# Performance work log

Hardware: AMD Instinct MI355X
Metric: run time of the kernel (lower is better)

## Reference

```python
import jax, jax.numpy as jnp
import numpy as np

E, I, H, T = 8, 2816, 1024, 8192

def setup_inputs() -> dict:
    key = jax.random.key(0)
    ks = jax.random.split(key, 5)
    scale_w = 1.0 / np.sqrt(H)
    return {
        "hidden_states": jax.random.normal(ks[0], (T, H), jnp.float32),
        "router_logits": jax.random.normal(ks[1], (T, E), jnp.float32),
        "W1": jax.random.normal(ks[2], (E, I, H), jnp.float32) * scale_w,
        "W3": jax.random.normal(ks[3], (E, I, H), jnp.float32) * scale_w,
        "W2": jax.random.normal(ks[4], (E, H, I), jnp.float32) * (1.0 / np.sqrt(I)),
        "top_k": 2,
    }

def reference(hidden_states, router_logits, W1, W3, W2, top_k):
    # softmax router in fp32, topk, renormalize (renormalize=True, use_grouped_topk=False)
    probs = jax.nn.softmax(router_logits.astype(jnp.float32), axis=-1)  # [T,E]
    vals, idx = jax.lax.top_k(probs, top_k)                             # [T,K]
    vals = vals / jnp.sum(vals, axis=-1, keepdims=True)
    vals = vals.astype(hidden_states.dtype)
    n_tok, n_exp = probs.shape
    # dense per-token expert weight matrix [T,E]; zero for unrouted experts,
    # mathematically identical to the gather/scatter-add in the ipex op
    w = jnp.zeros((n_tok, n_exp), hidden_states.dtype).at[
        jnp.arange(n_tok)[:, None], idx].add(vals)

    def expert_step(acc, args):
        We1, We3, We2, we = args  # [I,H], [I,H], [H,I], [T]
        h = jax.nn.silu(hidden_states @ We1.T) * (hidden_states @ We3.T)  # [T,I]
        return acc + we[:, None] * (h @ We2.T), None

    out, _ = jax.lax.scan(expert_step, jnp.zeros_like(hidden_states),
                          (W1, W3, W2, w.T))
    return out
```

## Files before the change

### kernel.cpp

```cpp
#include <hip/hip_runtime.h>
#include <stdint.h>

#define NE 8
#define NI 2816
#define NH 1024
#define NT 8192
#define NPAIR (NT * 2)

typedef __bf16 bf16x8 __attribute__((ext_vector_type(8)));
typedef float f32x4 __attribute__((ext_vector_type(4)));

__device__ __forceinline__ uint16_t f2bf(float f) {
    union { float f; uint32_t u; } v;
    v.f = f;
    return (uint16_t)((v.u + 0x7FFFu + ((v.u >> 16) & 1u)) >> 16);
}

__device__ __forceinline__ float bflo(uint32_t u) {
    union { uint32_t x; float f; } v; v.x = u << 16; return v.f;
}
__device__ __forceinline__ float bfhi(uint32_t u) {
    union { uint32_t x; float f; } v; v.x = u & 0xffff0000u; return v.f;
}

__device__ __forceinline__ void gld16(const void* g, void* l) {
    __builtin_amdgcn_global_load_lds(
        (__attribute__((address_space(1))) void*)(uintptr_t)g,
        (__attribute__((address_space(3))) void*)(uint32_t)(uintptr_t)l,
        16, 0, 0);
}

__global__ __launch_bounds__(256) void k_cvt_w13(const float* __restrict__ W1,
                                                 const float* __restrict__ W3,
                                                 uint16_t* __restrict__ Wg) {
    int row = blockIdx.x * 2 + (threadIdx.x >> 7);
    int g = threadIdx.x & 127;
    const float* src = (blockIdx.y == 0) ? W1 : W3;
    int e = row / NI;
    int r = row - e * NI;
    size_t drow = (size_t)e * (2 * NI) + (size_t)((r >> 4) * 32 + (r & 15) + (blockIdx.y ? 16 : 0));
    const float4* sp = (const float4*)(src + (size_t)row * NH);
    float4 a = sp[g * 2];
    float4 b = sp[g * 2 + 1];
    uint4 o;
    o.x = (uint32_t)f2bf(a.x) | ((uint32_t)f2bf(a.y) << 16);
    o.y = (uint32_t)f2bf(a.z) | ((uint32_t)f2bf(a.w) << 16);
    o.z = (uint32_t)f2bf(b.x) | ((uint32_t)f2bf(b.y) << 16);
    o.w = (uint32_t)f2bf(b.z) | ((uint32_t)f2bf(b.w) << 16);
    ((uint4*)(Wg + drow * NH))[g] = o;
}

__global__ __launch_bounds__(256) void k_cvt_flat(const float* __restrict__ S,
                                                  uint16_t* __restrict__ D) {
    size_t i = (size_t)blockIdx.x * 256 + threadIdx.x;
    float4 a = ((const float4*)S)[i * 2];
    float4 b = ((const float4*)S)[i * 2 + 1];
    uint4 o;
    o.x = (uint32_t)f2bf(a.x) | ((uint32_t)f2bf(a.y) << 16);
    o.y = (uint32_t)f2bf(a.z) | ((uint32_t)f2bf(a.w) << 16);
    o.z = (uint32_t)f2bf(b.x) | ((uint32_t)f2bf(b.y) << 16);
    o.w = (uint32_t)f2bf(b.z) | ((uint32_t)f2bf(b.w) << 16);
    ((uint4*)D)[i] = o;
}

__global__ __launch_bounds__(256) void k_router(const float* __restrict__ logits,
                                                int* __restrict__ tok_e,
                                                float2* __restrict__ tok_w,
                                                int* __restrict__ counts) {
    int t = blockIdx.x * 256 + threadIdx.x;
    if (t >= NT) return;
    float4 a = ((const float4*)logits)[(size_t)t * 2];
    float4 b = ((const float4*)logits)[(size_t)t * 2 + 1];
    float l[8] = {a.x, a.y, a.z, a.w, b.x, b.y, b.z, b.w};
    int i0 = 0; float l0 = l[0];
#pragma unroll
    for (int e = 1; e < 8; e++) if (l[e] > l0) { l0 = l[e]; i0 = e; }
    int i1 = -1; float l1 = -3.4e38f;
#pragma unroll
    for (int e = 0; e < 8; e++) if (e != i0 && l[e] > l1) { l1 = l[e]; i1 = e; }
    float w0 = 1.f / (1.f + __expf(l1 - l0));
    float w1 = 1.f - w0;
    tok_e[t] = i0 | (i1 << 8);
    tok_w[t] = make_float2(w0, w1);
    atomicAdd(&counts[i0], 1);
    atomicAdd(&counts[i1], 1);
}

__global__ void k_scan(const int* __restrict__ counts, int* __restrict__ offsets,
                       int* __restrict__ cursor) {
    if (threadIdx.x == 0) {
        int o = 0;
        for (int e = 0; e < NE; e++) { offsets[e] = o; cursor[e] = o; o += counts[e]; }
    }
}

__global__ __launch_bounds__(128) void k_gather(const float* __restrict__ x,
                                                const int* __restrict__ tok_e,
                                                const float2* __restrict__ tok_w,
                                                int* __restrict__ cursor,
                                                uint16_t* __restrict__ Xg,
                                                int2* __restrict__ tok_slots,
                                                float* __restrict__ slot_w) {
    int t = blockIdx.x;
    __shared__ int ss[2];
    if (threadIdx.x == 0) {
        int ee = tok_e[t];
        float2 w = tok_w[t];
        int s0 = atomicAdd(&cursor[ee & 0xff], 1);
        int s1 = atomicAdd(&cursor[(ee >> 8) & 0xff], 1);
        ss[0] = s0; ss[1] = s1;
        tok_slots[t] = make_int2(s0, s1);
        slot_w[s0] = w.x;
        slot_w[s1] = w.y;
    }
    __syncthreads();
    int s0 = ss[0], s1 = ss[1];
    int i = threadIdx.x;
    const float4* xr = (const float4*)(x + (size_t)t * NH);
    float4 a = xr[i * 2];
    float4 b = xr[i * 2 + 1];
    uint4 o;
    o.x = (uint32_t)f2bf(a.x) | ((uint32_t)f2bf(a.y) << 16);
    o.y = (uint32_t)f2bf(a.z) | ((uint32_t)f2bf(a.w) << 16);
    o.z = (uint32_t)f2bf(b.x) | ((uint32_t)f2bf(b.y) << 16);
    o.w = (uint32_t)f2bf(b.z) | ((uint32_t)f2bf(b.w) << 16);
    ((uint4*)(Xg + (size_t)s0 * NH))[i] = o;
    ((uint4*)(Xg + (size_t)s1 * NH))[i] = o;
}


#define BAR()  asm volatile("s_barrier" ::: "memory")
#define WAITLGKM0 asm volatile("s_waitcnt lgkmcnt(0)" ::: "memory")
#define WAITLGKM4 asm volatile("s_waitcnt lgkmcnt(4)" ::: "memory")
#define WAITV6 asm volatile("s_waitcnt vmcnt(6)" ::: "memory")
#define WAITV0 asm volatile("s_waitcnt vmcnt(0)" ::: "memory")
#define SCHB __builtin_amdgcn_sched_barrier(0)
#define PRIO1 __builtin_amdgcn_s_setprio(1)
#define PRIO0 __builtin_amdgcn_s_setprio(0)

#define STAGE(ab, bufsel, h, kt)                                                  \
    do {                                                                          \
        char* d_ = lds + (bufsel) * 65536 + (ab) * 32768 + (h) * 16384 + tid * 16; \
        gld16(((ab) ? srcB : srcA)[h][0] + (kt) * 64, d_);                         \
        gld16(((ab) ? srcB : srcA)[h][1] + (kt) * 64, d_ + 8192);                  \
    } while (0)

#define READA(bufsel, mh)                                                           \
    do {                                                                            \
        _Pragma("unroll") for (int ii = 0; ii < 4; ii++) {                          \
            const char* p_ = lds + (bufsel) * 65536 + wr * 16384 +                  \
                             (((mh) * 4 + ii) * 16 + l15) * 128;                    \
            af[ii][0] = *(const bf16x8*)(p_ + colk0);                               \
            af[ii][1] = *(const bf16x8*)(p_ + colk1);                               \
        }                                                                           \
    } while (0)

#define READB(bufsel, nh, dst)                                                      \
    do {                                                                            \
        _Pragma("unroll") for (int jj = 0; jj < 2; jj++) {                          \
            int gb_ = wc * 64 + ((nh) * 2 + jj) * 16;                               \
            const char* p_ = lds + (bufsel) * 65536 + 32768 + (gb_ >> 7) * 16384 +  \
                             ((gb_ & 127) + l15) * 128;                             \
            dst[jj][0] = *(const bf16x8*)(p_ + colk0);                              \
            dst[jj][1] = *(const bf16x8*)(p_ + colk1);                              \
        }                                                                           \
    } while (0)

#define MMQ(mh, bsrc, jb)                                                           \
    do {                                                                            \
        _Pragma("unroll") for (int ii = 0; ii < 4; ii++)                            \
            _Pragma("unroll") for (int jj = 0; jj < 2; jj++)                        \
                _Pragma("unroll") for (int ks = 0; ks < 2; ks++)                    \
                    acc[(mh) * 4 + ii][(jb) + jj] =                                 \
                        __builtin_amdgcn_mfma_f32_16x16x32_bf16(                    \
                            af[ii][ks], bsrc[jj][ks], acc[(mh) * 4 + ii][(jb) + jj],\
                            0, 0, 0);                                               \
    } while (0)

template <int MODE>
__global__ __launch_bounds__(512, 2) void k_moe_gemm(const uint16_t* __restrict__ Abase,
                                                     const uint16_t* __restrict__ Bbase,
                                                     uint16_t* __restrict__ Cbase,
                                                     const int* __restrict__ counts,
                                                     const int* __restrict__ offsets) {
    constexpr int K = (MODE == 1) ? NH : NI;
    constexpr int NKT = K / 64;
    constexpr int NITER = NKT / 2;
    constexpr int BROWS = (MODE == 1) ? 2 * NI : NH;
    constexpr int CLD = (MODE == 1) ? NI : NH;

    int e = blockIdx.z;
    int n_e = counts[e];
    int mtile = blockIdx.y;
    if (mtile * 256 >= n_e) return;
    int ntile = blockIdx.x;
    int off = offsets[e];

    __shared__ __align__(16) char lds[131072];

    int tid = threadIdx.x;
    int l15 = tid & 15;
    int q = (tid >> 4) & 3;
    int x7 = tid & 7;
    int wv = tid >> 6, wr = wv >> 2, wc = wv & 3;
    int colk0 = (q ^ x7) << 4;
    int colk1 = ((q + 4) ^ x7) << 4;

    int sr = tid >> 3;
    int ss = x7 ^ (sr & 7);
    const uint16_t* srcA[2][2];
    const uint16_t* srcB[2][2];
#pragma unroll
    for (int h = 0; h < 2; h++)
#pragma unroll
        for (int j = 0; j < 2; j++) {
            int gr = off + mtile * 256 + h * 128 + j * 64 + sr;
            gr = min(gr, NPAIR - 1);
            srcA[h][j] = Abase + (size_t)gr * K + ss * 8;
            int gn = ntile * 256 + h * 128 + j * 64 + sr;
            srcB[h][j] = Bbase + (size_t)e * BROWS * K + (size_t)gn * K + ss * 8;
        }

    bf16x8 af[4][2], b0[2][2], b1[2][2];
    f32x4 acc[8][4] = {};

    STAGE(1, 0, 0, 0);
    STAGE(1, 0, 1, 0);
    STAGE(0, 0, 0, 0);
    STAGE(0, 0, 1, 0);
    STAGE(1, 1, 0, 1);
    STAGE(1, 1, 1, 1);
    STAGE(0, 1, 0, 1);
    WAITV6;
    BAR();

#pragma unroll 1
    for (int it = 0; it < NITER; ++it) {
        int kt1 = 2 * it + 1;
        int kt2 = min(2 * it + 2, NKT - 1);
        int kt3 = min(2 * it + 3, NKT - 1);
        READA(0, 0);
        READB(0, 0, b0);
        READB(0, 1, b1);
        STAGE(0, 1, 1, kt1);
        WAITLGKM4; SCHB; PRIO1; MMQ(0, b0, 0); PRIO0; SCHB;
        BAR();
        STAGE(1, 0, 0, kt2);
        WAITLGKM0; SCHB; PRIO1; MMQ(0, b1, 2); PRIO0; SCHB;
        READA(0, 1);
        BAR();
        STAGE(1, 0, 1, kt2);
        WAITLGKM0; SCHB; PRIO1; MMQ(1, b1, 2); PRIO0; SCHB;
        BAR();
        STAGE(0, 0, 0, kt2);
        PRIO1; MMQ(1, b0, 0); PRIO0; SCHB;
        WAITV6;
        BAR();
        READA(1, 0);
        READB(1, 0, b0);
        READB(1, 1, b1);
        STAGE(0, 0, 1, kt2);
        WAITLGKM4; SCHB; PRIO1; MMQ(0, b0, 0); PRIO0; SCHB;
        BAR();
        STAGE(1, 1, 0, kt3);
        WAITLGKM0; SCHB; PRIO1; MMQ(0, b1, 2); PRIO0; SCHB;
        READA(1, 1);
        BAR();
        STAGE(1, 1, 1, kt3);
        WAITLGKM0; SCHB; PRIO1; MMQ(1, b1, 2); PRIO0; SCHB;
        BAR();
        STAGE(0, 1, 0, kt3);
        PRIO1; MMQ(1, b0, 0); PRIO0; SCHB;
        WAITV6;
        BAR();
    }

    WAITV0;

    int sBase = off + mtile * 256;
    if constexpr (MODE == 1) {
#pragma unroll
        for (int im = 0; im < 8; im++) {
#pragma unroll
            for (int r = 0; r < 4; r++) {
                int lm = wr * 128 + im * 16 + q * 4 + r;
                if (mtile * 256 + lm < n_e) {
                    uint16_t* orow = Cbase + (size_t)(sBase + lm) * CLD +
                                     ntile * 128 + wc * 32 + l15;
#pragma unroll
                    for (int j = 0; j < 2; j++) {
                        float c1 = acc[im][2 * j][r];
                        float c3 = acc[im][2 * j + 1][r];
                        float hv = (c1 / (1.f + __expf(-c1))) * c3;
                        orow[j * 16] = f2bf(hv);
                    }
                }
            }
        }
    } else {
#pragma unroll
        for (int im = 0; im < 8; im++) {
#pragma unroll
            for (int r = 0; r < 4; r++) {
                int lm = wr * 128 + im * 16 + q * 4 + r;
                if (mtile * 256 + lm < n_e) {
                    uint16_t* orow = Cbase + (size_t)(sBase + lm) * CLD +
                                     ntile * 256 + wc * 64 + l15;
#pragma unroll
                    for (int jn = 0; jn < 4; jn++) orow[jn * 16] = f2bf(acc[im][jn][r]);
                }
            }
        }
    }
}

__global__ __launch_bounds__(256) void k_combine(const uint16_t* __restrict__ Y,
                                                 const int2* __restrict__ tok_slots,
                                                 const float* __restrict__ slot_w,
                                                 float* __restrict__ out) {
    int idx = blockIdx.x * 256 + threadIdx.x;
    int t = idx >> 7;
    int g = idx & 127;
    int2 s = tok_slots[t];
    float w0 = slot_w[s.x], w1 = slot_w[s.y];
    uint4 u0 = ((const uint4*)(Y + (size_t)s.x * NH))[g];
    uint4 u1 = ((const uint4*)(Y + (size_t)s.y * NH))[g];
    float4 o0, o1;
    o0.x = w0 * bflo(u0.x) + w1 * bflo(u1.x);
    o0.y = w0 * bfhi(u0.x) + w1 * bfhi(u1.x);
    o0.z = w0 * bflo(u0.y) + w1 * bflo(u1.y);
    o0.w = w0 * bfhi(u0.y) + w1 * bfhi(u1.y);
    o1.x = w0 * bflo(u0.z) + w1 * bflo(u1.z);
    o1.y = w0 * bfhi(u0.z) + w1 * bfhi(u1.z);
    o1.z = w0 * bflo(u0.w) + w1 * bflo(u1.w);
    o1.w = w0 * bfhi(u0.w) + w1 * bfhi(u1.w);
    float4* orow = (float4*)(out + (size_t)t * NH + g * 8);
    orow[0] = o0;
    orow[1] = o1;
}

extern "C" void kernel_launch(void* const* d_in, const int* in_sizes, int n_in,
                              void* d_out, int out_size, void* d_ws, size_t ws_size,
                              hipStream_t stream) {
    const float* x = (const float*)d_in[0];
    const float* logits = (const float*)d_in[1];
    const float* W1 = (const float*)d_in[2];
    const float* W3 = (const float*)d_in[3];
    const float* W2 = (const float*)d_in[4];
    float* out = (float*)d_out;

    char* ws = (char*)d_ws;
    size_t o = 0;
    auto nxt = [&](size_t b) -> void* {
        void* p = ws + o;
        o += (b + 255) & ~(size_t)255;
        return p;
    };
    const size_t WELEMS = (size_t)NE * NI * NH;
    uint16_t* Wg = (uint16_t*)nxt(WELEMS * 2 * 2);
    uint16_t* W2b = (uint16_t*)nxt(WELEMS * 2);
    uint16_t* Xg = (uint16_t*)nxt((size_t)NPAIR * NH * 2);
    uint16_t* Hbuf = (uint16_t*)nxt((size_t)NPAIR * NI * 2);
    float* slot_w = (float*)nxt((size_t)NPAIR * 4);
    int2* tok_slots = (int2*)nxt((size_t)NT * 8);
    int* tok_e = (int*)nxt((size_t)NT * 4);
    float2* tok_w = (float2*)nxt((size_t)NT * 8);
    int* meta = (int*)nxt(128);
    int* counts = meta;
    int* offsets = meta + 8;
    int* cursor = meta + 16;
    uint16_t* Ybuf = Xg;
    (void)ws_size; (void)in_sizes; (void)n_in;

    hipMemsetAsync(meta, 0, 128, stream);

    k_router<<<NT / 256, 256, 0, stream>>>(logits, tok_e, tok_w, counts);
    k_scan<<<1, 64, 0, stream>>>(counts, offsets, cursor);

    k_cvt_w13<<<dim3(NE * NI / 2, 2), 256, 0, stream>>>(W1, W3, Wg);
    k_cvt_flat<<<(unsigned)(WELEMS / 8 / 256), 256, 0, stream>>>(W2, W2b);

    k_gather<<<NT, 128, 0, stream>>>(x, tok_e, tok_w, cursor, Xg, tok_slots, slot_w);

    k_moe_gemm<1><<<dim3(2 * NI / 256, NT / 256, NE), 512, 0, stream>>>(
        Xg, Wg, Hbuf, counts, offsets);
    k_moe_gemm<2><<<dim3(NH / 256, NT / 256, NE), 512, 0, stream>>>(
        Hbuf, W2b, Ybuf, counts, offsets);

    k_combine<<<NT * NH / 8 / 256, 256, 0, stream>>>(Ybuf, tok_slots, slot_w, out);
}
```

Measured before the change: 885.9 us.

## Split MoE GEMMs, give down-projection a smaller 64-row tile and remap block order

```diff
diff --git a/kernel.cpp b/kernel.cpp
--- a/kernel.cpp
+++ b/kernel.cpp
@@ -133,6 +133,7 @@
 #define WAITLGKM0 asm volatile("s_waitcnt lgkmcnt(0)" ::: "memory")
 #define WAITLGKM4 asm volatile("s_waitcnt lgkmcnt(4)" ::: "memory")
 #define WAITV6 asm volatile("s_waitcnt vmcnt(6)" ::: "memory")
+#define WAITV2 asm volatile("s_waitcnt vmcnt(2)" ::: "memory")
 #define WAITV0 asm volatile("s_waitcnt vmcnt(0)" ::: "memory")
 #define SCHB __builtin_amdgcn_sched_barrier(0)
 #define PRIO1 __builtin_amdgcn_s_setprio(1)
@@ -177,23 +178,28 @@
                             0, 0, 0);                                               \
     } while (0)
 
-template <int MODE>
-__global__ __launch_bounds__(512, 2) void k_moe_gemm(const uint16_t* __restrict__ Abase,
-                                                     const uint16_t* __restrict__ Bbase,
-                                                     uint16_t* __restrict__ Cbase,
-                                                     const int* __restrict__ counts,
-                                                     const int* __restrict__ offsets) {
-    constexpr int K = (MODE == 1) ? NH : NI;
+__global__ __launch_bounds__(512, 2) void k_gemm1(const uint16_t* __restrict__ Abase,
+                                                  const uint16_t* __restrict__ Bbase,
+                                                  uint16_t* __restrict__ Cbase,
+                                                  const int* __restrict__ counts,
+                                                  const int* __restrict__ offsets) {
+    constexpr int K = NH;
     constexpr int NKT = K / 64;
     constexpr int NITER = NKT / 2;
-    constexpr int BROWS = (MODE == 1) ? 2 * NI : NH;
-    constexpr int CLD = (MODE == 1) ? NI : NH;
-
-    int e = blockIdx.z;
+    constexpr int BROWS = 2 * NI;
+    constexpr int CLD = NI;
+    constexpr int GX = 2 * NI / 256, GY = NT / 256;
+    constexpr int CPX = GX * GY * NE / 8;
+
+    int lin = blockIdx.x + GX * (blockIdx.y + GY * blockIdx.z);
+    int w = (lin & 7) * CPX + (lin >> 3);
+    int ntile = w % GX;
+    int rem = w / GX;
+    int mtile = rem % GY;
+    int e = rem / GY;
+
     int n_e = counts[e];
-    int mtile = blockIdx.y;
     if (mtile * 256 >= n_e) return;
-    int ntile = blockIdx.x;
     int off = offsets[e];
 
     __shared__ __align__(16) char lds[131072];
@@ -278,37 +284,160 @@
     WAITV0;
 
     int sBase = off + mtile * 256;
-    if constexpr (MODE == 1) {
-#pragma unroll
-        for (int im = 0; im < 8; im++) {
-#pragma unroll
-            for (int r = 0; r < 4; r++) {
-                int lm = wr * 128 + im * 16 + q * 4 + r;
-                if (mtile * 256 + lm < n_e) {
-                    uint16_t* orow = Cbase + (size_t)(sBase + lm) * CLD +
-                                     ntile * 128 + wc * 32 + l15;
-#pragma unroll
-                    for (int j = 0; j < 2; j++) {
-                        float c1 = acc[im][2 * j][r];
-                        float c3 = acc[im][2 * j + 1][r];
-                        float hv = (c1 / (1.f + __expf(-c1))) * c3;
-                        orow[j * 16] = f2bf(hv);
-                    }
+#pragma unroll
+    for (int im = 0; im < 8; im++) {
+#pragma unroll
+        for (int r = 0; r < 4; r++) {
+            int lm = wr * 128 + im * 16 + q * 4 + r;
+            if (mtile * 256 + lm < n_e) {
+                uint16_t* orow = Cbase + (size_t)(sBase + lm) * CLD +
+                                 ntile * 128 + wc * 32 + l15;
+#pragma unroll
+                for (int j = 0; j < 2; j++) {
+                    float c1 = acc[im][2 * j][r];
+                    float c3 = acc[im][2 * j + 1][r];
+                    float hv = (c1 / (1.f + __expf(-c1))) * c3;
+                    orow[j * 16] = f2bf(hv);
                 }
             }
         }
-    } else {
-#pragma unroll
-        for (int im = 0; im < 8; im++) {
-#pragma unroll
-            for (int r = 0; r < 4; r++) {
-                int lm = wr * 128 + im * 16 + q * 4 + r;
-                if (mtile * 256 + lm < n_e) {
-                    uint16_t* orow = Cbase + (size_t)(sBase + lm) * CLD +
-                                     ntile * 256 + wc * 64 + l15;
-#pragma unroll
-                    for (int jn = 0; jn < 4; jn++) orow[jn * 16] = f2bf(acc[im][jn][r]);
-                }
+    }
+}
+
+
+#define G2STAGE_A(s, kt)                                                     \
+    do {                                                                     \
+        char* d_ = lds2 + (s) * 40960 + tid * 16;                            \
+        gld16(pA0 + (kt) * 64, d_);                                          \
+        gld16(pA1 + (kt) * 64, d_ + 4096);                                   \
+    } while (0)
+#define G2STAGE_BH(s, h, kt)                                                 \
+    do {                                                                     \
+        char* d_ = lds2 + (s) * 40960 + 8192 + (h) * 16384 + tid * 16;       \
+        gld16(pB[(h) * 4 + 0] + (kt) * 64, d_);                              \
+        gld16(pB[(h) * 4 + 1] + (kt) * 64, d_ + 4096);                       \
+        gld16(pB[(h) * 4 + 2] + (kt) * 64, d_ + 8192);                       \
+        gld16(pB[(h) * 4 + 3] + (kt) * 64, d_ + 12288);                      \
+    } while (0)
+#define G2READA(s)                                                           \
+    do {                                                                     \
+        _Pragma("unroll") for (int ii = 0; ii < 4; ii++) {                   \
+            const char* p_ = lds2 + (s) * 40960 + (ii * 16 + l15) * 128;     \
+            af[ii][0] = *(const bf16x8*)(p_ + colk0);                        \
+            af[ii][1] = *(const bf16x8*)(p_ + colk1);                        \
+        }                                                                    \
+    } while (0)
+#define G2READB(s, h)                                                        \
+    do {                                                                     \
+        _Pragma("unroll") for (int jj = 0; jj < 2; jj++) {                   \
+            const char* p_ = lds2 + (s) * 40960 + 8192 +                     \
+                             (wv * 64 + ((h) * 2 + jj) * 16 + l15) * 128;    \
+            bf[(h) * 2 + jj][0] = *(const bf16x8*)(p_ + colk0);              \
+            bf[(h) * 2 + jj][1] = *(const bf16x8*)(p_ + colk1);              \
+        }                                                                    \
+    } while (0)
+#define G2MMQ(h)                                                             \
+    do {                                                                     \
+        _Pragma("unroll") for (int ii = 0; ii < 4; ii++)                     \
+            _Pragma("unroll") for (int jj = 0; jj < 2; jj++)                 \
+                _Pragma("unroll") for (int ks = 0; ks < 2; ks++)             \
+                    acc[ii][(h) * 2 + jj] =                                  \
+                        __builtin_amdgcn_mfma_f32_16x16x32_bf16(             \
+                            af[ii][ks], bf[(h) * 2 + jj][ks],                \
+                            acc[ii][(h) * 2 + jj], 0, 0, 0);                 \
+    } while (0)
+
+__global__ __launch_bounds__(256, 2) void k_gemm2b(const uint16_t* __restrict__ Hbuf,
+                                                   const uint16_t* __restrict__ W2b,
+                                                   uint16_t* __restrict__ Ybuf,
+                                                   const int* __restrict__ counts,
+                                                   const int* __restrict__ offsets) {
+    constexpr int K = NI;
+    constexpr int NKT = K / 64;
+    constexpr int NITER = NKT / 2;
+    constexpr int GX = NT / 64, GY = NH / 256;
+    constexpr int CPX = GX * GY * NE / 8;
+
+    int lin = blockIdx.x + GX * (blockIdx.y + GY * blockIdx.z);
+    int w = (lin & 7) * CPX + (lin >> 3);
+    int mtile = w % GX;
+    int rem = w / GX;
+    int ntile = rem % GY;
+    int e = rem / GY;
+
+    int n_e = counts[e];
+    if (mtile * 64 >= n_e) return;
+    int off = offsets[e];
+
+    __shared__ __align__(16) char lds2[81920];
+
+    int tid = threadIdx.x;
+    int l15 = tid & 15;
+    int q = (tid >> 4) & 3;
+    int x7 = tid & 7;
+    int wv = tid >> 6;
+    int colk0 = (q ^ x7) << 4;
+    int colk1 = ((q + 4) ^ x7) << 4;
+
+    int sr = tid >> 3;
+    int ss = x7 ^ (sr & 7);
+    int ra0 = min(off + mtile * 64 + sr, NPAIR - 1);
+    int ra1 = min(off + mtile * 64 + 32 + sr, NPAIR - 1);
+    const uint16_t* pA0 = Hbuf + (size_t)ra0 * K + ss * 8;
+    const uint16_t* pA1 = Hbuf + (size_t)ra1 * K + ss * 8;
+    const uint16_t* pB[8];
+#pragma unroll
+    for (int j = 0; j < 8; j++)
+        pB[j] = W2b + ((size_t)e * NH + ntile * 256 + j * 32 + sr) * K + ss * 8;
+
+    bf16x8 af[4][2], bf[4][2];
+    f32x4 acc[4][4] = {};
+
+    G2STAGE_A(0, 0);
+    G2STAGE_BH(0, 0, 0);
+    G2STAGE_BH(0, 1, 0);
+    G2STAGE_A(1, 1);
+    WAITV2;
+    BAR();
+
+#pragma unroll 1
+    for (int it = 0; it < NITER; ++it) {
+        int kt1 = 2 * it + 1;
+        int kt2 = min(2 * it + 2, NKT - 1);
+        int kt3 = min(2 * it + 3, NKT - 1);
+        G2READA(0); G2READB(0, 0); G2READB(0, 1);
+        G2STAGE_BH(1, 0, kt1);
+        WAITLGKM4; SCHB; PRIO1; G2MMQ(0); PRIO0; SCHB;
+        BAR();
+        G2STAGE_BH(1, 1, kt1);
+        G2STAGE_A(0, kt2);
+        WAITLGKM0; SCHB; PRIO1; G2MMQ(1); PRIO0; SCHB;
+        WAITV2;
+        BAR();
+        G2READA(1); G2READB(1, 0); G2READB(1, 1);
+        G2STAGE_BH(0, 0, kt2);
+        WAITLGKM4; SCHB; PRIO1; G2MMQ(0); PRIO0; SCHB;
+        BAR();
+        G2STAGE_BH(0, 1, kt2);
+        G2STAGE_A(1, kt3);
+        WAITLGKM0; SCHB; PRIO1; G2MMQ(1); PRIO0; SCHB;
+        WAITV2;
+        BAR();
+    }
+
+    WAITV0;
+
+    int sBase = off + mtile * 64;
+#pragma unroll
+    for (int im = 0; im < 4; im++) {
+#pragma unroll
+        for (int r = 0; r < 4; r++) {
+            int lm = im * 16 + q * 4 + r;
+            if (mtile * 64 + lm < n_e) {
+                uint16_t* orow = Ybuf + (size_t)(sBase + lm) * NH +
+                                 ntile * 256 + wv * 64 + l15;
+#pragma unroll
+                for (int jn = 0; jn < 4; jn++) orow[jn * 16] = f2bf(acc[im][jn][r]);
             }
         }
     }
@@ -382,9 +511,9 @@
 
     k_gather<<<NT, 128, 0, stream>>>(x, tok_e, tok_w, cursor, Xg, tok_slots, slot_w);
 
-    k_moe_gemm<1><<<dim3(2 * NI / 256, NT / 256, NE), 512, 0, stream>>>(
+    k_gemm1<<<dim3(2 * NI / 256, NT / 256, NE), 512, 0, stream>>>(
         Xg, Wg, Hbuf, counts, offsets);
-    k_moe_gemm<2><<<dim3(NH / 256, NT / 256, NE), 512, 0, stream>>>(
+    k_gemm2b<<<dim3(NT / 64, NH / 256, NE), 256, 0, stream>>>(
         Hbuf, W2b, Ybuf, counts, offsets);
 
     k_combine<<<NT * NH / 8 / 256, 256, 0, stream>>>(Ybuf, tok_slots, slot_w, out);
```

Result: slower. 925.5 us (+4.5%).
